# Kernel optimization log

Hardware: AMD Instinct MI355X
Metric: run time of the kernel (lower is better)

Reference implementation:

```python
import jax, jax.numpy as jnp
import numpy as np

D = 256; HEADS = 8; LEVELS = 4; POINTS = 4; DFFN = 1024
B = 8; NQ = 300; NC = 16
SPATIAL = [(64, 64), (32, 32), (16, 16), (8, 8)]  # (H, W) per feature level (static)
LEN_IN = sum(h * w for h, w in SPATIAL)  # 5440
EPS = 1e-5


def layer_norm(x, w, b):
    m = x.mean(-1, keepdims=True)
    v = ((x - m) ** 2).mean(-1, keepdims=True)
    return (x - m) * jax.lax.rsqrt(v + EPS) * w + b


def mha(q, k, v, in_w, in_b, out_w, out_b):
    # torch nn.MultiheadAttention with packed qkv in_proj. q,k,v: [b, s, D]
    b, s, _ = q.shape
    dh = D // HEADS
    wq, wk, wv = jnp.split(in_w, 3, axis=0)
    bq, bk, bv = jnp.split(in_b, 3)
    proj = lambda x, w, bb: (x @ w.T + bb).reshape(b, s, HEADS, dh).transpose(0, 2, 1, 3)
    qh, kh, vh = proj(q, wq, bq), proj(k, wk, bk), proj(v, wv, bv)
    attn = jax.nn.softmax(jnp.einsum('bhqd,bhkd->bhqk', qh / np.sqrt(dh), kh), axis=-1)
    o = jnp.einsum('bhqk,bhkd->bhqd', attn, vh).transpose(0, 2, 1, 3).reshape(b, s, D)
    return o @ out_w.T + out_b


def bilinear_sample(value_l, loc, H_, W_):
    # value_l: [b, heads, H_*W_, dh]; loc: [b, heads, lq, P, 2] normalized to [0,1]
    # matches F.grid_sample(mode='bilinear', padding_mode='zeros', align_corners=False)
    b, nh, lq, p, _ = loc.shape
    dh = value_l.shape[-1]
    x = loc[..., 0] * W_ - 0.5
    y = loc[..., 1] * H_ - 0.5
    x0f = jnp.floor(x); y0f = jnp.floor(y)
    lx = x - x0f; ly = y - y0f
    x0 = x0f.astype(jnp.int32); y0 = y0f.astype(jnp.int32)
    def gather(xi, yi, w):
        valid = (xi >= 0) & (xi < W_) & (yi >= 0) & (yi < H_)
        idx = jnp.clip(yi, 0, H_ - 1) * W_ + jnp.clip(xi, 0, W_ - 1)
        vals = jnp.take_along_axis(value_l, idx.reshape(b, nh, lq * p, 1), axis=2)
        return vals.reshape(b, nh, lq, p, dh) * (w * valid)[..., None]
    out = gather(x0, y0, (1 - lx) * (1 - ly))
    out = out + gather(x0 + 1, y0, lx * (1 - ly))
    out = out + gather(x0, y0 + 1, (1 - lx) * ly)
    out = out + gather(x0 + 1, y0 + 1, lx * ly)
    return out  # [b, heads, lq, P, dh]


def ms_deform_attn(query, ref_pts, src, pad_mask, value_w, value_b, off_w, off_b, attw_w, attw_b, out_w, out_b):
    b, lq, _ = query.shape
    dh = D // HEADS
    value = src @ value_w.T + value_b
    value = jnp.where(pad_mask[..., None], 0.0, value)
    value = value.reshape(b, LEN_IN, HEADS, dh).transpose(0, 2, 1, 3)  # [b,H,Len,dh]
    off = (query @ off_w.T + off_b).reshape(b, lq, HEADS, LEVELS, POINTS, 2)
    aw = jax.nn.softmax((query @ attw_w.T + attw_b).reshape(b, lq, HEADS, LEVELS * POINTS), axis=-1)
    aw = aw.reshape(b, lq, HEADS, LEVELS, POINTS).transpose(0, 2, 1, 3, 4)  # [b,H,lq,L,P]
    norm = jnp.array([[w_, h_] for h_, w_ in SPATIAL], dtype=query.dtype)  # (W, H) per level
    loc = ref_pts[:, :, None, :, None, :] + off / norm[None, None, None, :, None, :]
    loc = loc.transpose(0, 2, 1, 3, 4, 5)  # [b,H,lq,L,P,2]
    out = jnp.zeros((b, HEADS, lq, dh), query.dtype)
    start = 0
    for l, (H_, W_) in enumerate(SPATIAL):
        v_l = jax.lax.dynamic_slice_in_dim(value, start, H_ * W_, axis=2)
        s = bilinear_sample(v_l, loc[:, :, :, l], H_, W_)
        out = out + (s * aw[:, :, :, l, :, None]).sum(3)
        start += H_ * W_
    out = out.transpose(0, 2, 1, 3).reshape(b, lq, D)
    return out @ out_w.T + out_b


def setup_inputs():
    ks = iter(jax.random.split(jax.random.key(0), 64))
    w = lambda *shape: jax.random.normal(next(ks), shape, jnp.float32) * 0.02
    return {
        'tgt': jax.random.normal(next(ks), (B, NQ, NC, D), jnp.float32),
        'query_pos': jax.random.normal(next(ks), (B, NQ, NC, D), jnp.float32),
        'reference_points': jax.random.uniform(next(ks), (B, NQ * NC, LEVELS, 2), jnp.float32),
        'src': jax.random.normal(next(ks), (B, LEN_IN, D), jnp.float32),
        'src_spatial_shapes': jnp.array(SPATIAL, jnp.int32),
        'level_start_index': jnp.array(np.cumsum([0] + [h * ww for h, ww in SPATIAL[:-1]]), jnp.int32),
        'src_padding_mask': jnp.zeros((B, LEN_IN), bool),
        'sa_in_w': w(3 * D, D), 'sa_in_b': jnp.zeros(3 * D, jnp.float32),
        'sa_out_w': w(D, D), 'sa_out_b': jnp.zeros(D, jnp.float32),
        'norm2_w': jnp.ones(D, jnp.float32), 'norm2_b': jnp.zeros(D, jnp.float32),
        'ca_value_w': w(D, D), 'ca_value_b': jnp.zeros(D, jnp.float32),
        'ca_off_w': w(HEADS * LEVELS * POINTS * 2, D), 'ca_off_b': w(HEADS * LEVELS * POINTS * 2),
        'ca_attw_w': w(HEADS * LEVELS * POINTS, D), 'ca_attw_b': jnp.zeros(HEADS * LEVELS * POINTS, jnp.float32),
        'ca_out_w': w(D, D), 'ca_out_b': jnp.zeros(D, jnp.float32),
        'norm1_w': jnp.ones(D, jnp.float32), 'norm1_b': jnp.zeros(D, jnp.float32),
        'lin1_w': w(DFFN, D), 'lin1_b': jnp.zeros(DFFN, jnp.float32),
        'lin2_w': w(D, DFFN), 'lin2_b': jnp.zeros(D, jnp.float32),
        'norm3_w': jnp.ones(D, jnp.float32), 'norm3_b': jnp.zeros(D, jnp.float32),
    }


def _forward(tgt, query_pos, reference_points, src, pad_mask, sa_in_w, sa_in_b, sa_out_w, sa_out_b, norm2_w, norm2_b, ca_value_w, ca_value_b, ca_off_w, ca_off_b, ca_attw_w, ca_attw_b, ca_out_w, ca_out_b, norm1_w, norm1_b, lin1_w, lin1_b, lin2_w, lin2_b, norm3_w, norm3_b):
    b, nq, nc, dm = tgt.shape
    # point-to-point self-attention within each contour (batch folded with queries)
    t = tgt.reshape(b * nq, nc, dm)
    qp = query_pos.reshape(b * nq, nc, dm)
    q = t + qp
    t2 = mha(q, q, t, sa_in_w, sa_in_b, sa_out_w, sa_out_b)
    t = layer_norm(t + t2, norm2_w, norm2_b)
    # multi-scale deformable cross-attention over flattened feature pyramid
    t = t.reshape(b, nq * nc, dm)
    qp = qp.reshape(b, nq * nc, dm)
    t2 = ms_deform_attn(t + qp, reference_points, src, pad_mask, ca_value_w, ca_value_b, ca_off_w, ca_off_b, ca_attw_w, ca_attw_b, ca_out_w, ca_out_b)
    t = layer_norm(t + t2, norm1_w, norm1_b)
    # FFN (dropout is identity in eval)
    t2 = jax.nn.relu(t @ lin1_w.T + lin1_b) @ lin2_w.T + lin2_b
    t = layer_norm(t + t2, norm3_w, norm3_b)
    return t.reshape(b, nq, nc, dm)


def reference(tgt, query_pos, reference_points, src, src_spatial_shapes, level_start_index, src_padding_mask, sa_in_w, sa_in_b, sa_out_w, sa_out_b, norm2_w, norm2_b, ca_value_w, ca_value_b, ca_off_w, ca_off_b, ca_attw_w, ca_attw_b, ca_out_w, ca_out_b, norm1_w, norm1_b, lin1_w, lin1_b, lin2_w, lin2_b, norm3_w, norm3_b):
    # src_spatial_shapes / level_start_index are static (SPATIAL); accepted for API fidelity
    return _forward(tgt, query_pos, reference_points, src, src_padding_mask, sa_in_w, sa_in_b, sa_out_w, sa_out_b, norm2_w, norm2_b, ca_value_w, ca_value_b, ca_off_w, ca_off_b, ca_attw_w, ca_attw_b, ca_out_w, ca_out_b, norm1_w, norm1_b, lin1_w, lin1_b, lin2_w, lin2_b, norm3_w, norm3_b)
```

## Files before the change

kernel.cpp:

```cpp
#include <hip/hip_runtime.h>


typedef __bf16 bf16x8 __attribute__((ext_vector_type(8)));
typedef float  f32x4  __attribute__((ext_vector_type(4)));
typedef float  f32x2  __attribute__((ext_vector_type(2)));

__device__ __forceinline__ unsigned pk_bf16(float lo, float hi)
{
    unsigned a = __float_as_uint(lo) + 0x8000u;
    unsigned b = __float_as_uint(hi) + 0x8000u;
    return __builtin_amdgcn_perm(b, a, 0x07060302u);
}
__device__ __forceinline__ unsigned short f2bf(float v)
{
    return (unsigned short)((__float_as_uint(v) + 0x8000u) >> 16);
}
__device__ __forceinline__ float bf_lo(unsigned u) { return __uint_as_float(u << 16); }
__device__ __forceinline__ float bf_hi(unsigned u) { return __uint_as_float(u & 0xffff0000u); }
__device__ __forceinline__ float bf1(unsigned short u) { return __uint_as_float((unsigned)u << 16); }
__device__ __forceinline__ f32x2 bfpair(unsigned u)
{
    f32x2 r;
    r.x = __uint_as_float(u << 16);
    r.y = __uint_as_float(u & 0xffff0000u);
    return r;
}

struct WcvtArgs {
    const float* src[8];
    unsigned short* dst[8];
    int n4[8];
};

__global__ __launch_bounds__(256) void wcvt(WcvtArgs a)
{
    const int gid = blockIdx.x * 256 + threadIdx.x;
    const int stride = gridDim.x * 256;
#pragma unroll
    for (int s = 0; s < 8; s++) {
        const float4* sp = (const float4*)a.src[s];
        uint2* dp = (uint2*)a.dst[s];
        for (int i = gid; i < a.n4[s]; i += stride) {
            float4 f = sp[i];
            uint2 o; o.x = pk_bf16(f.x, f.y); o.y = pk_bf16(f.z, f.w);
            dp[i] = o;
        }
    }
}

template <int ABF16>
__device__ __forceinline__ void gemm_core64(
    const void* __restrict__ Xv, const float* __restrict__ Y,
    const unsigned short* __restrict__ Wb, const float* __restrict__ bias,
    void* __restrict__ Cv, int outbf16, int relu,
    int row0, int col0, int N, int K,
    unsigned short (*sA)[64][40], unsigned short (*sB)[128][40])
{
    const int tid  = threadIdx.x;
    const int lane = tid & 63;
    const int wv   = tid >> 6;
    const int wr   = wv >> 1;
    const int wc   = wv & 1;
    const int lm   = lane & 15;
    const int ko   = (lane >> 4) << 3;
    const int q4   = (lane >> 4) << 2;

    const int ar  = tid >> 2;
    const int ash = (tid & 3) << 3;
    const int br  = tid >> 1;
    const int bsh = (tid & 1) << 4;

    const unsigned short* Ab = (const unsigned short*)Xv;
    const float* Af = (const float*)Xv;

    f32x4 acc[2][4] = {};
    uint4 ra, rb0, rb1;

    const int iters = K >> 5;

    auto load_k = [&](int k) {
        if (ABF16) {
            ra = *(const uint4*)(Ab + (size_t)(row0 + ar) * K + k + ash);
        } else {
            const float* Ar = Af + (size_t)(row0 + ar) * K + k + ash;
            float4 f0 = ((const float4*)Ar)[0];
            float4 f1 = ((const float4*)Ar)[1];
            if (Y) {
                const float* Yr = Y + (size_t)(row0 + ar) * K + k + ash;
                float4 g0 = ((const float4*)Yr)[0];
                float4 g1 = ((const float4*)Yr)[1];
                f0.x += g0.x; f0.y += g0.y; f0.z += g0.z; f0.w += g0.w;
                f1.x += g1.x; f1.y += g1.y; f1.z += g1.z; f1.w += g1.w;
            }
            ra.x = pk_bf16(f0.x, f0.y); ra.y = pk_bf16(f0.z, f0.w);
            ra.z = pk_bf16(f1.x, f1.y); ra.w = pk_bf16(f1.z, f1.w);
        }
        const unsigned short* Wr = Wb + (size_t)(col0 + br) * K + k + bsh;
        rb0 = ((const uint4*)Wr)[0];
        rb1 = ((const uint4*)Wr)[1];
    };
    auto store_k = [&](int buf) {
        *(uint4*)&sA[buf][ar][ash]     = ra;
        *(uint4*)&sB[buf][br][bsh]     = rb0;
        *(uint4*)&sB[buf][br][bsh + 8] = rb1;
    };

    load_k(0);
    store_k(0);

    for (int it = 0; it < iters; ++it) {
        __syncthreads();
        const int buf = it & 1;
        if (it + 1 < iters) load_k((it + 1) << 5);

        bf16x8 av[2], bv[4];
#pragma unroll
        for (int mi = 0; mi < 2; mi++)
            av[mi] = *(const bf16x8*)&sA[buf][wr * 32 + mi * 16 + lm][ko];
#pragma unroll
        for (int ni = 0; ni < 4; ni++)
            bv[ni] = *(const bf16x8*)&sB[buf][wc * 64 + ni * 16 + lm][ko];
#pragma unroll
        for (int mi = 0; mi < 2; mi++)
#pragma unroll
            for (int ni = 0; ni < 4; ni++)
                acc[mi][ni] = __builtin_amdgcn_mfma_f32_16x16x32_bf16(
                    av[mi], bv[ni], acc[mi][ni], 0, 0, 0);

        if (it + 1 < iters) store_k(buf ^ 1);
    }

#pragma unroll
    for (int ni = 0; ni < 4; ni++) {
        const int col = col0 + wc * 64 + ni * 16 + lm;
        const float bsv = bias[col];
#pragma unroll
        for (int mi = 0; mi < 2; mi++) {
            const int rowb = row0 + wr * 32 + mi * 16 + q4;
#pragma unroll
            for (int rr = 0; rr < 4; rr++) {
                float v = acc[mi][ni][rr] + bsv;
                if (relu) v = fmaxf(v, 0.f);
                if (outbf16)
                    ((unsigned short*)Cv)[(size_t)(rowb + rr) * N + col] = f2bf(v);
                else
                    ((float*)Cv)[(size_t)(rowb + rr) * N + col] = v;
            }
        }
    }
}

template <int ABF16>
__global__ __launch_bounds__(256) void gemm_std64(
    const void* __restrict__ Xv, const float* __restrict__ Y,
    const unsigned short* __restrict__ Wb, const float* __restrict__ bias,
    void* __restrict__ Cv, int outbf16, int relu, int N, int K)
{
    __shared__ unsigned short sA[2][64][40];
    __shared__ unsigned short sB[2][128][40];
    gemm_core64<ABF16>(Xv, Y, Wb, bias, Cv, outbf16, relu,
                       blockIdx.y * 64, blockIdx.x * 128, N, K, sA, sB);
}

__global__ __launch_bounds__(256) void gemm_qkvval(
    const float* __restrict__ tgt, const float* __restrict__ qpos,
    const unsigned short* __restrict__ Wsa, const float* __restrict__ bsa,
    unsigned short* __restrict__ qkB, unsigned short* __restrict__ vB,
    const float* __restrict__ src,
    const unsigned short* __restrict__ Wval, const float* __restrict__ bval,
    unsigned short* __restrict__ valB)
{
    __shared__ unsigned short sA[2][64][40];
    __shared__ unsigned short sB[2][128][40];
    const int x = blockIdx.x, y = blockIdx.y;
    if (x < 4) {
        if (y >= 600) return;
        gemm_core64<0>(tgt, qpos, Wsa, bsa, qkB, 1, 0, y * 64, x * 128, 512, 256, sA, sB);
    } else if (x < 6) {
        if (y >= 600) return;
        gemm_core64<0>(tgt, nullptr, Wsa + 512 * 256, bsa + 512, vB, 1, 0,
                       y * 64, (x - 4) * 128, 256, 256, sA, sB);
    } else {
        gemm_core64<0>(src, nullptr, Wval, bval, valB, 1, 0,
                       y * 64, (x - 6) * 128, 256, 256, sA, sB);
    }
}

__global__ __launch_bounds__(256) void gemm_offaw(
    const unsigned short* __restrict__ X,
    const unsigned short* __restrict__ Woff, const float* __restrict__ boff,
    unsigned short* __restrict__ offB,
    const unsigned short* __restrict__ Watt, const float* __restrict__ batt,
    float* __restrict__ awL)
{
    __shared__ unsigned short sA[2][64][40];
    __shared__ unsigned short sB[2][128][40];
    if (blockIdx.x >= 2)
        gemm_core64<1>(X, nullptr, Watt, batt, awL, 0, 0,
                       blockIdx.y * 64, 0, 128, 256, sA, sB);
    else
        gemm_core64<1>(X, nullptr, Woff, boff, offB, 1, 0,
                       blockIdx.y * 64, blockIdx.x * 128, 256, 256, sA, sB);
}

__global__ __launch_bounds__(256) void attn16(
    const unsigned short* __restrict__ QK, const unsigned short* __restrict__ V,
    unsigned short* __restrict__ O)
{
    __shared__ unsigned short sqk[16][520];
    __shared__ unsigned short sv[16][264];
    __shared__ float sp[128][17];

    const int g = blockIdx.x;
    const int tid = threadIdx.x;

    const uint4* qg = (const uint4*)(QK + (size_t)g * 8192);
    for (int i = tid; i < 1024; i += 256)
        *(uint4*)&sqk[i >> 6][(i & 63) * 8] = qg[i];
    const uint4* vg = (const uint4*)(V + (size_t)g * 4096);
    for (int i = tid; i < 512; i += 256)
        *(uint4*)&sv[i >> 5][(i & 31) * 8] = vg[i];
    __syncthreads();

#pragma unroll 2
    for (int s = tid; s < 2048; s += 256) {
        const int h = s >> 8, qi = (s >> 4) & 15, kj = s & 15;
        const uint4* qp = (const uint4*)&sqk[qi][h * 32];
        const uint4* kp = (const uint4*)&sqk[kj][256 + h * 32];
        float acc = 0.f;
#pragma unroll
        for (int c = 0; c < 4; c++) {
            uint4 qu = qp[c];
            uint4 ku = kp[c];
            acc += bf_lo(qu.x) * bf_lo(ku.x) + bf_hi(qu.x) * bf_hi(ku.x)
                 + bf_lo(qu.y) * bf_lo(ku.y) + bf_hi(qu.y) * bf_hi(ku.y)
                 + bf_lo(qu.z) * bf_lo(ku.z) + bf_hi(qu.z) * bf_hi(ku.z)
                 + bf_lo(qu.w) * bf_lo(ku.w) + bf_hi(qu.w) * bf_hi(ku.w);
        }
        sp[s >> 4][s & 15] = acc * 0.17677669529663687f;
    }
    __syncthreads();

    if (tid < 128) {
        float* row = sp[tid];
        float mx = row[0];
#pragma unroll
        for (int j = 1; j < 16; j++) mx = fmaxf(mx, row[j]);
        float sum = 0.f;
#pragma unroll
        for (int j = 0; j < 16; j++) { float e = __expf(row[j] - mx); row[j] = e; sum += e; }
        float inv = 1.f / sum;
#pragma unroll
        for (int j = 0; j < 16; j++) row[j] *= inv;
    }
    __syncthreads();

    uint2* og = (uint2*)(O + (size_t)g * 4096);
    for (int o = tid; o < 1024; o += 256) {
        const int qi = o >> 6, cq = o & 63, h = cq >> 3;
        const float* pr = sp[h * 16 + qi];
        float a0 = 0.f, a1 = 0.f, a2 = 0.f, a3 = 0.f;
#pragma unroll
        for (int j = 0; j < 16; j++) {
            uint2 u = *(const uint2*)&sv[j][cq * 4];
            float p = pr[j];
            a0 += p * bf_lo(u.x); a1 += p * bf_hi(u.x);
            a2 += p * bf_lo(u.y); a3 += p * bf_hi(u.y);
        }
        uint2 r; r.x = pk_bf16(a0, a1); r.y = pk_bf16(a2, a3);
        og[o] = r;
    }
}

template <int XBF16, int WRITE2, int ADDQ>
__global__ __launch_bounds__(256) void ln_res4(
    const void* __restrict__ Xv, const float* __restrict__ R,
    const float* __restrict__ w, const float* __restrict__ b,
    float* __restrict__ out, unsigned short* __restrict__ out2,
    const float* __restrict__ qpos)
{
    const int row = blockIdx.x * 4 + (threadIdx.x >> 6);
    const int lane = threadIdx.x & 63;
    const size_t base = (size_t)row * 256 + lane * 4;

    float x0, x1, x2, x3;
    if (XBF16) {
        uint2 u = *(const uint2*)((const unsigned short*)Xv + base);
        x0 = bf_lo(u.x); x1 = bf_hi(u.x); x2 = bf_lo(u.y); x3 = bf_hi(u.y);
    } else {
        float4 f = *(const float4*)((const float*)Xv + base);
        x0 = f.x; x1 = f.y; x2 = f.z; x3 = f.w;
    }
    float4 r4 = *(const float4*)&R[base];
    float v0 = x0 + r4.x, v1 = x1 + r4.y, v2 = x2 + r4.z, v3 = x3 + r4.w;

    float s = v0 + v1 + v2 + v3;
#pragma unroll
    for (int o = 32; o > 0; o >>= 1) s += __shfl_xor(s, o);
    const float mean = s * (1.f / 256.f);
    const float d0 = v0 - mean, d1 = v1 - mean, d2 = v2 - mean, d3 = v3 - mean;
    float q = d0 * d0 + d1 * d1 + d2 * d2 + d3 * d3;
#pragma unroll
    for (int o = 32; o > 0; o >>= 1) q += __shfl_xor(q, o);
    const float rs = rsqrtf(q * (1.f / 256.f) + 1e-5f);

    float4 w4 = *(const float4*)&w[lane * 4];
    float4 b4 = *(const float4*)&b[lane * 4];
    float y0 = d0 * rs * w4.x + b4.x;
    float y1 = d1 * rs * w4.y + b4.y;
    float y2 = d2 * rs * w4.z + b4.z;
    float y3 = d3 * rs * w4.w + b4.w;

    float4 o4; o4.x = y0; o4.y = y1; o4.z = y2; o4.w = y3;
    *(float4*)&out[base] = o4;
    if (WRITE2) {
        float z0 = y0, z1 = y1, z2 = y2, z3 = y3;
        if (ADDQ) {
            float4 qp4 = *(const float4*)&qpos[base];
            z0 += qp4.x; z1 += qp4.y; z2 += qp4.z; z3 += qp4.w;
        }
        uint2 u; u.x = pk_bf16(z0, z1); u.y = pk_bf16(z2, z3);
        *(uint2*)(out2 + base) = u;
    }
}

__global__ __launch_bounds__(256) void ms_sample4(
    const unsigned short* __restrict__ VAL, const unsigned short* __restrict__ OFF,
    const float* __restrict__ AWL, const float* __restrict__ REF,
    unsigned short* __restrict__ OUT)
{
    __shared__ unsigned short soff[1024];
    __shared__ float saw[512];
    __shared__ float sref[32];
    __shared__ float swt[4][16][8][4];
    __shared__ int   sidx[4][16][8][4];

    const int m0 = blockIdx.x * 4, tid = threadIdx.x;

    ((uint2*)soff)[tid] = ((const uint2*)(OFF + (size_t)m0 * 256))[tid];
    ((float2*)saw)[tid] = ((const float2*)(AWL + (size_t)m0 * 128))[tid];
    if (tid < 32) sref[tid] = REF[(size_t)m0 * 8 + tid];
    __syncthreads();

    if (tid < 32) {
        float* row = &saw[tid * 16];
        float mx = row[0];
#pragma unroll
        for (int j = 1; j < 16; j++) mx = fmaxf(mx, row[j]);
        float s = 0.f, e[16];
#pragma unroll
        for (int j = 0; j < 16; j++) { e[j] = __expf(row[j] - mx); s += e[j]; }
        float inv = 1.f / s;
#pragma unroll
        for (int j = 0; j < 16; j++) row[j] = e[j] * inv;
    }
    __syncthreads();

    for (int c = tid; c < 512; c += 256) {
        const int qi = c >> 7, h = c & 7, j = (c >> 3) & 15;
        const int l = j >> 2, p = j & 3;
        const int Wl = 64 >> l;
        const int st = (l == 0) ? 0 : (l == 1) ? 4096 : (l == 2) ? 5120 : 5376;
        const float fS = (float)Wl;
        const unsigned short* ob = &soff[qi * 256 + h * 32 + l * 8 + p * 2];
        const float x = sref[qi * 8 + l * 2 + 0] * fS + bf1(ob[0]) - 0.5f;
        const float y = sref[qi * 8 + l * 2 + 1] * fS + bf1(ob[1]) - 0.5f;
        const float x0f = floorf(x), y0f = floorf(y);
        const float fx = x - x0f, fy = y - y0f;
        const int x0 = (int)x0f, y0 = (int)y0f;
        const int x1 = x0 + 1, y1 = y0 + 1;
        const float vx0 = (x0 >= 0 && x0 < Wl) ? 1.f : 0.f;
        const float vx1 = (x1 >= 0 && x1 < Wl) ? 1.f : 0.f;
        const float vy0 = (y0 >= 0 && y0 < Wl) ? 1.f : 0.f;
        const float vy1 = (y1 >= 0 && y1 < Wl) ? 1.f : 0.f;
        const int cx0 = min(max(x0, 0), Wl - 1);
        const int cx1 = min(max(x1, 0), Wl - 1);
        const int cy0 = min(max(y0, 0), Wl - 1);
        const int cy1 = min(max(y1, 0), Wl - 1);
        const float aw = saw[qi * 128 + h * 16 + j];
        float4 w4;
        w4.x = (1.f - fx) * (1.f - fy) * vx0 * vy0 * aw;
        w4.y = fx * (1.f - fy) * vx1 * vy0 * aw;
        w4.z = (1.f - fx) * fy * vx0 * vy1 * aw;
        w4.w = fx * fy * vx1 * vy1 * aw;
        int4 i4;
        i4.x = (st + cy0 * Wl + cx0) << 9;
        i4.y = (st + cy0 * Wl + cx1) << 9;
        i4.z = (st + cy1 * Wl + cx0) << 9;
        i4.w = (st + cy1 * Wl + cx1) << 9;
        *(float4*)&swt[qi][j][h][0] = w4;
        *(int4*)&sidx[qi][j][h][0]  = i4;
    }
    __syncthreads();

    const int qi = tid >> 6, lane = tid & 63, h = lane >> 3;
    const int m = m0 + qi, bb = m / 4800;
    const char* vb = (const char*)VAL + (size_t)bb * 5440 * 512 + lane * 8;

    f32x2 a01 = {0.f, 0.f}, a23 = {0.f, 0.f};
#pragma unroll 4
    for (int j = 0; j < 16; j++) {
        const float4 w = *(const float4*)&swt[qi][j][h][0];
        const int4  id = *(const int4*)&sidx[qi][j][h][0];
        uint2 c0 = *(const uint2*)(vb + id.x);
        uint2 c1 = *(const uint2*)(vb + id.y);
        uint2 c2 = *(const uint2*)(vb + id.z);
        uint2 c3 = *(const uint2*)(vb + id.w);
        a01 += w.x * bfpair(c0.x) + w.y * bfpair(c1.x)
             + w.z * bfpair(c2.x) + w.w * bfpair(c3.x);
        a23 += w.x * bfpair(c0.y) + w.y * bfpair(c1.y)
             + w.z * bfpair(c2.y) + w.w * bfpair(c3.y);
    }
    uint2 o;
    o.x = pk_bf16(a01.x, a01.y);
    o.y = pk_bf16(a23.x, a23.y);
    *(uint2*)(OUT + (size_t)m * 256 + lane * 4) = o;
}

extern "C" void kernel_launch(void* const* d_in, const int* in_sizes, int n_in,
                              void* d_out, int out_size, void* d_ws, size_t ws_size,
                              hipStream_t stream)
{
    const float* tgt        = (const float*)d_in[0];
    const float* qpos       = (const float*)d_in[1];
    const float* refp       = (const float*)d_in[2];
    const float* src        = (const float*)d_in[3];
    const float* sa_in_w    = (const float*)d_in[7];
    const float* sa_in_b    = (const float*)d_in[8];
    const float* sa_out_w   = (const float*)d_in[9];
    const float* sa_out_b   = (const float*)d_in[10];
    const float* norm2_w    = (const float*)d_in[11];
    const float* norm2_b    = (const float*)d_in[12];
    const float* ca_value_w = (const float*)d_in[13];
    const float* ca_value_b = (const float*)d_in[14];
    const float* ca_off_w   = (const float*)d_in[15];
    const float* ca_off_b   = (const float*)d_in[16];
    const float* ca_attw_w  = (const float*)d_in[17];
    const float* ca_attw_b  = (const float*)d_in[18];
    const float* ca_out_w   = (const float*)d_in[19];
    const float* ca_out_b   = (const float*)d_in[20];
    const float* norm1_w    = (const float*)d_in[21];
    const float* norm1_b    = (const float*)d_in[22];
    const float* lin1_w     = (const float*)d_in[23];
    const float* lin1_b     = (const float*)d_in[24];
    const float* lin2_w     = (const float*)d_in[25];
    const float* lin2_b     = (const float*)d_in[26];
    const float* norm3_w    = (const float*)d_in[27];
    const float* norm3_b    = (const float*)d_in[28];
    float* out = (float*)d_out;

    const int M1 = 38400;
    float* ws = (float*)d_ws;
    float* A  = ws;
    float* Bx = A  + 9830400;
    float* Cx = Bx + 4915200;
    float* Dx = Cx + 4915200;
    float* Ex = Dx + 4915200;
    float* Fx = Ex + 5570560;
    float* Gx = Fx + 19660800;

    unsigned short* qkB   = (unsigned short*)A;
    float*          t1    = A;
    float*          t2    = A;
    unsigned short* vB    = (unsigned short*)Bx;
    unsigned short* t1qB  = (unsigned short*)Bx;
    unsigned short* sampB = (unsigned short*)Bx;
    unsigned short* l2B   = (unsigned short*)Bx;
    unsigned short* aoB   = (unsigned short*)Cx;
    unsigned short* offB  = (unsigned short*)Cx;
    unsigned short* coB   = (unsigned short*)Cx;
    unsigned short* t2B   = (unsigned short*)Cx;
    unsigned short* soB   = (unsigned short*)Dx;
    float*          awL   = Dx;
    unsigned short* valB  = (unsigned short*)Ex;
    unsigned short* hidB  = (unsigned short*)Fx;
    unsigned short* wG    = (unsigned short*)Gx;

    unsigned short* wSAIN  = wG;
    unsigned short* wSAOUT = wG + 196608;
    unsigned short* wVAL   = wG + 262144;
    unsigned short* wOFF   = wG + 327680;
    unsigned short* wATT   = wG + 393216;
    unsigned short* wCAOUT = wG + 425984;
    unsigned short* wL1    = wG + 491520;
    unsigned short* wL2    = wG + 753664;

    dim3 blk(256);

    WcvtArgs wa;
    wa.src[0] = sa_in_w;    wa.dst[0] = wSAIN;  wa.n4[0] = 196608 / 4;
    wa.src[1] = sa_out_w;   wa.dst[1] = wSAOUT; wa.n4[1] = 65536 / 4;
    wa.src[2] = ca_value_w; wa.dst[2] = wVAL;   wa.n4[2] = 65536 / 4;
    wa.src[3] = ca_off_w;   wa.dst[3] = wOFF;   wa.n4[3] = 65536 / 4;
    wa.src[4] = ca_attw_w;  wa.dst[4] = wATT;   wa.n4[4] = 32768 / 4;
    wa.src[5] = ca_out_w;   wa.dst[5] = wCAOUT; wa.n4[5] = 65536 / 4;
    wa.src[6] = lin1_w;     wa.dst[6] = wL1;    wa.n4[6] = 262144 / 4;
    wa.src[7] = lin2_w;     wa.dst[7] = wL2;    wa.n4[7] = 262144 / 4;
    wcvt<<<512, blk, 0, stream>>>(wa);

    gemm_qkvval<<<dim3(8, 680), blk, 0, stream>>>(tgt, qpos, wSAIN, sa_in_b, qkB, vB,
                                                  src, wVAL, ca_value_b, valB);
    attn16<<<2400, blk, 0, stream>>>(qkB, vB, aoB);
    gemm_std64<1><<<dim3(2, 600), blk, 0, stream>>>(aoB, nullptr, wSAOUT, sa_out_b, soB, 1, 0, 256, 256);
    ln_res4<1, 1, 1><<<9600, blk, 0, stream>>>(soB, tgt, norm2_w, norm2_b, t1, t1qB, qpos);

    gemm_offaw<<<dim3(3, 600), blk, 0, stream>>>(t1qB, wOFF, ca_off_b, offB, wATT, ca_attw_b, awL);
    ms_sample4<<<9600, blk, 0, stream>>>(valB, offB, awL, refp, sampB);
    gemm_std64<1><<<dim3(2, 600), blk, 0, stream>>>(sampB, nullptr, wCAOUT, ca_out_b, coB, 1, 0, 256, 256);
    ln_res4<1, 1, 0><<<9600, blk, 0, stream>>>(coB, t1, norm1_w, norm1_b, t2, t2B, nullptr);

    gemm_std64<1><<<dim3(8, 600), blk, 0, stream>>>(t2B, nullptr, wL1, lin1_b, hidB, 1, 1, 1024, 256);
    gemm_std64<1><<<dim3(2, 600), blk, 0, stream>>>(hidB, nullptr, wL2, lin2_b, l2B, 1, 0, 256, 1024);
    ln_res4<1, 0, 0><<<9600, blk, 0, stream>>>(l2B, t2, norm3_w, norm3_b, out, nullptr, nullptr);
}
```

Before: 589.5 us.

## Replace tiled GEMMs with A-stationary row-block GEMM streaming weights from global

Replaces the double-buffered 64x128 LDS-tiled GEMM with a kernel that stages a 64-row slab of A (256-wide K chunk) in shared memory once, keeps it in registers, and loops over output column groups while loading B fragments directly from global/L2. This removes repeated A re-reads across column blocks and most of the per-k synchronisation, and cuts grid size to one block per row slab. In exchange, weights are read uncached by LDS per wave with less latency hiding, each wave handles only 16 rows, and blocks serialize over column groups, reducing parallelism.

After: 1.080 ms. 1.83x slower.

```diff
diff --git a/kernel.cpp b/kernel.cpp
--- a/kernel.cpp
+++ b/kernel.cpp
@@ -48,98 +48,66 @@
     }
 }
 
-template <int ABF16>
-__device__ __forceinline__ void gemm_core64(
+template <int ABF16, int NF, int KC>
+__device__ __forceinline__ void gemm_astat(
     const void* __restrict__ Xv, const float* __restrict__ Y,
     const unsigned short* __restrict__ Wb, const float* __restrict__ bias,
     void* __restrict__ Cv, int outbf16, int relu,
-    int row0, int col0, int N, int K,
-    unsigned short (*sA)[64][40], unsigned short (*sB)[128][40])
+    int row0, int N, int groups, unsigned short (*sA)[264])
 {
     const int tid  = threadIdx.x;
     const int lane = tid & 63;
     const int wv   = tid >> 6;
-    const int wr   = wv >> 1;
-    const int wc   = wv & 1;
     const int lm   = lane & 15;
     const int ko   = (lane >> 4) << 3;
     const int q4   = (lane >> 4) << 2;
-
-    const int ar  = tid >> 2;
-    const int ash = (tid & 3) << 3;
-    const int br  = tid >> 1;
-    const int bsh = (tid & 1) << 4;
-
-    const unsigned short* Ab = (const unsigned short*)Xv;
-    const float* Af = (const float*)Xv;
-
-    f32x4 acc[2][4] = {};
-    uint4 ra, rb0, rb1;
-
-    const int iters = K >> 5;
-
-    auto load_k = [&](int k) {
+    const int K    = KC * 256;
+
+    const int arow = tid >> 2;
+    const int aseg = tid & 3;
+
+    auto stage = [&](int kc) {
+        uint4* dst = (uint4*)&sA[arow][aseg * 64];
         if (ABF16) {
-            ra = *(const uint4*)(Ab + (size_t)(row0 + ar) * K + k + ash);
+            const uint4* Ar = (const uint4*)((const unsigned short*)Xv +
+                              (size_t)(row0 + arow) * K + kc * 256 + aseg * 64);
+#pragma unroll
+            for (int i = 0; i < 8; i++) {
+                const int j = (i + aseg) & 7;
+                dst[j] = Ar[j];
+            }
         } else {
-            const float* Ar = Af + (size_t)(row0 + ar) * K + k + ash;
-            float4 f0 = ((const float4*)Ar)[0];
-            float4 f1 = ((const float4*)Ar)[1];
-            if (Y) {
-                const float* Yr = Y + (size_t)(row0 + ar) * K + k + ash;
-                float4 g0 = ((const float4*)Yr)[0];
-                float4 g1 = ((const float4*)Yr)[1];
-                f0.x += g0.x; f0.y += g0.y; f0.z += g0.z; f0.w += g0.w;
-                f1.x += g1.x; f1.y += g1.y; f1.z += g1.z; f1.w += g1.w;
+            const float* Ar = (const float*)Xv + (size_t)(row0 + arow) * 256 + aseg * 64;
+            const float* Yr = Y ? (Y + (size_t)(row0 + arow) * 256 + aseg * 64) : nullptr;
+#pragma unroll
+            for (int i = 0; i < 8; i++) {
+                const int j = (i + aseg) & 7;
+                float4 f0 = ((const float4*)Ar)[2 * j];
+                float4 f1 = ((const float4*)Ar)[2 * j + 1];
+                if (Y) {
+                    float4 g0 = ((const float4*)Yr)[2 * j];
+                    float4 g1 = ((const float4*)Yr)[2 * j + 1];
+                    f0.x += g0.x; f0.y += g0.y; f0.z += g0.z; f0.w += g0.w;
+                    f1.x += g1.x; f1.y += g1.y; f1.z += g1.z; f1.w += g1.w;
+                }
+                uint4 u;
+                u.x = pk_bf16(f0.x, f0.y); u.y = pk_bf16(f0.z, f0.w);
+                u.z = pk_bf16(f1.x, f1.y); u.w = pk_bf16(f1.z, f1.w);
+                dst[j] = u;
             }
-            ra.x = pk_bf16(f0.x, f0.y); ra.y = pk_bf16(f0.z, f0.w);
-            ra.z = pk_bf16(f1.x, f1.y); ra.w = pk_bf16(f1.z, f1.w);
-        }
-        const unsigned short* Wr = Wb + (size_t)(col0 + br) * K + k + bsh;
-        rb0 = ((const uint4*)Wr)[0];
-        rb1 = ((const uint4*)Wr)[1];
+        }
     };
-    auto store_k = [&](int buf) {
-        *(uint4*)&sA[buf][ar][ash]     = ra;
-        *(uint4*)&sB[buf][br][bsh]     = rb0;
-        *(uint4*)&sB[buf][br][bsh + 8] = rb1;
-    };
-
-    load_k(0);
-    store_k(0);
-
-    for (int it = 0; it < iters; ++it) {
-        __syncthreads();
-        const int buf = it & 1;
-        if (it + 1 < iters) load_k((it + 1) << 5);
-
-        bf16x8 av[2], bv[4];
-#pragma unroll
-        for (int mi = 0; mi < 2; mi++)
-            av[mi] = *(const bf16x8*)&sA[buf][wr * 32 + mi * 16 + lm][ko];
-#pragma unroll
-        for (int ni = 0; ni < 4; ni++)
-            bv[ni] = *(const bf16x8*)&sB[buf][wc * 64 + ni * 16 + lm][ko];
-#pragma unroll
-        for (int mi = 0; mi < 2; mi++)
-#pragma unroll
-            for (int ni = 0; ni < 4; ni++)
-                acc[mi][ni] = __builtin_amdgcn_mfma_f32_16x16x32_bf16(
-                    av[mi], bv[ni], acc[mi][ni], 0, 0, 0);
-
-        if (it + 1 < iters) store_k(buf ^ 1);
-    }
-
-#pragma unroll
-    for (int ni = 0; ni < 4; ni++) {
-        const int col = col0 + wc * 64 + ni * 16 + lm;
-        const float bsv = bias[col];
-#pragma unroll
-        for (int mi = 0; mi < 2; mi++) {
-            const int rowb = row0 + wr * 32 + mi * 16 + q4;
+
+    const int rowb = row0 + wv * 16 + q4;
+
+    auto epi = [&](f32x4* acc, int colg) {
+#pragma unroll
+        for (int nf = 0; nf < NF; nf++) {
+            const int col = colg + nf * 16 + lm;
+            const float bsv = bias[col];
 #pragma unroll
             for (int rr = 0; rr < 4; rr++) {
-                float v = acc[mi][ni][rr] + bsv;
+                float v = acc[nf][rr] + bsv;
                 if (relu) v = fmaxf(v, 0.f);
                 if (outbf16)
                     ((unsigned short*)Cv)[(size_t)(rowb + rr) * N + col] = f2bf(v);
@@ -147,19 +115,69 @@
                     ((float*)Cv)[(size_t)(rowb + rr) * N + col] = v;
             }
         }
-    }
-}
-
-template <int ABF16>
-__global__ __launch_bounds__(256) void gemm_std64(
+    };
+
+    if (KC == 1) {
+        stage(0);
+        __syncthreads();
+        bf16x8 av[8];
+#pragma unroll
+        for (int ks = 0; ks < 8; ks++)
+            av[ks] = *(const bf16x8*)&sA[wv * 16 + lm][ks * 32 + ko];
+
+        for (int g = 0; g < groups; g++) {
+            const int colg = g * (NF * 16);
+            f32x4 acc[NF] = {};
+#pragma unroll
+            for (int nf = 0; nf < NF; nf++) {
+                const unsigned short* Wr = Wb + (size_t)(colg + nf * 16 + lm) * K + ko;
+                bf16x8 bv[8];
+#pragma unroll
+                for (int ks = 0; ks < 8; ks++)
+                    bv[ks] = *(const bf16x8*)(Wr + ks * 32);
+#pragma unroll
+                for (int ks = 0; ks < 8; ks++)
+                    acc[nf] = __builtin_amdgcn_mfma_f32_16x16x32_bf16(
+                        av[ks], bv[ks], acc[nf], 0, 0, 0);
+            }
+            epi(acc, colg);
+        }
+    } else {
+        f32x4 acc[NF] = {};
+        for (int kc = 0; kc < KC; kc++) {
+            if (kc) __syncthreads();
+            stage(kc);
+            __syncthreads();
+            bf16x8 av[8];
+#pragma unroll
+            for (int ks = 0; ks < 8; ks++)
+                av[ks] = *(const bf16x8*)&sA[wv * 16 + lm][ks * 32 + ko];
+#pragma unroll
+            for (int nf = 0; nf < NF; nf++) {
+                const unsigned short* Wr = Wb + (size_t)(nf * 16 + lm) * K + kc * 256 + ko;
+                bf16x8 bv[8];
+#pragma unroll
+                for (int ks = 0; ks < 8; ks++)
+                    bv[ks] = *(const bf16x8*)(Wr + ks * 32);
+#pragma unroll
+                for (int ks = 0; ks < 8; ks++)
+                    acc[nf] = __builtin_amdgcn_mfma_f32_16x16x32_bf16(
+                        av[ks], bv[ks], acc[nf], 0, 0, 0);
+            }
+        }
+        epi(acc, 0);
+    }
+}
+
+template <int ABF16, int NF, int KC>
+__global__ __launch_bounds__(256) void gemm_one(
     const void* __restrict__ Xv, const float* __restrict__ Y,
     const unsigned short* __restrict__ Wb, const float* __restrict__ bias,
-    void* __restrict__ Cv, int outbf16, int relu, int N, int K)
-{
-    __shared__ unsigned short sA[2][64][40];
-    __shared__ unsigned short sB[2][128][40];
-    gemm_core64<ABF16>(Xv, Y, Wb, bias, Cv, outbf16, relu,
-                       blockIdx.y * 64, blockIdx.x * 128, N, K, sA, sB);
+    void* __restrict__ Cv, int outbf16, int relu, int N, int groups)
+{
+    __shared__ unsigned short sA[64][264];
+    gemm_astat<ABF16, NF, KC>(Xv, Y, Wb, bias, Cv, outbf16, relu,
+                              blockIdx.x * 64, N, groups, sA);
 }
 
 __global__ __launch_bounds__(256) void gemm_qkvval(
@@ -170,20 +188,16 @@
     const unsigned short* __restrict__ Wval, const float* __restrict__ bval,
     unsigned short* __restrict__ valB)
 {
-    __shared__ unsigned short sA[2][64][40];
-    __shared__ unsigned short sB[2][128][40];
-    const int x = blockIdx.x, y = blockIdx.y;
-    if (x < 4) {
-        if (y >= 600) return;
-        gemm_core64<0>(tgt, qpos, Wsa, bsa, qkB, 1, 0, y * 64, x * 128, 512, 256, sA, sB);
-    } else if (x < 6) {
-        if (y >= 600) return;
-        gemm_core64<0>(tgt, nullptr, Wsa + 512 * 256, bsa + 512, vB, 1, 0,
-                       y * 64, (x - 4) * 128, 256, 256, sA, sB);
-    } else {
-        gemm_core64<0>(src, nullptr, Wval, bval, valB, 1, 0,
-                       y * 64, (x - 6) * 128, 256, 256, sA, sB);
-    }
+    __shared__ unsigned short sA[64][264];
+    const int b = blockIdx.x;
+    if (b < 600)
+        gemm_astat<0, 8, 1>(tgt, qpos, Wsa, bsa, qkB, 1, 0, b * 64, 512, 4, sA);
+    else if (b < 1200)
+        gemm_astat<0, 8, 1>(tgt, nullptr, Wsa + 512 * 256, bsa + 512, vB, 1, 0,
+                            (b - 600) * 64, 256, 2, sA);
+    else
+        gemm_astat<0, 8, 1>(src, nullptr, Wval, bval, valB, 1, 0,
+                            (b - 1200) * 64, 256, 2, sA);
 }
 
 __global__ __launch_bounds__(256) void gemm_offaw(
@@ -193,14 +207,12 @@
     const unsigned short* __restrict__ Watt, const float* __restrict__ batt,
     float* __restrict__ awL)
 {
-    __shared__ unsigned short sA[2][64][40];
-    __shared__ unsigned short sB[2][128][40];
-    if (blockIdx.x >= 2)
-        gemm_core64<1>(X, nullptr, Watt, batt, awL, 0, 0,
-                       blockIdx.y * 64, 0, 128, 256, sA, sB);
+    __shared__ unsigned short sA[64][264];
+    const int b = blockIdx.x;
+    if (b < 600)
+        gemm_astat<1, 8, 1>(X, nullptr, Woff, boff, offB, 1, 0, b * 64, 256, 2, sA);
     else
-        gemm_core64<1>(X, nullptr, Woff, boff, offB, 1, 0,
-                       blockIdx.y * 64, blockIdx.x * 128, 256, 256, sA, sB);
+        gemm_astat<1, 8, 1>(X, nullptr, Watt, batt, awL, 0, 0, (b - 600) * 64, 128, 1, sA);
 }
 
 __global__ __launch_bounds__(256) void attn16(
@@ -449,7 +461,6 @@
     const float* norm3_b    = (const float*)d_in[28];
     float* out = (float*)d_out;
 
-    const int M1 = 38400;
     float* ws = (float*)d_ws;
     float* A  = ws;
     float* Bx = A  + 9830400;
@@ -498,18 +509,18 @@
     wa.src[7] = lin2_w;     wa.dst[7] = wL2;    wa.n4[7] = 262144 / 4;
     wcvt<<<512, blk, 0, stream>>>(wa);
 
-    gemm_qkvval<<<dim3(8, 680), blk, 0, stream>>>(tgt, qpos, wSAIN, sa_in_b, qkB, vB,
-                                                  src, wVAL, ca_value_b, valB);
+    gemm_qkvval<<<1880, blk, 0, stream>>>(tgt, qpos, wSAIN, sa_in_b, qkB, vB,
+                                          src, wVAL, ca_value_b, valB);
     attn16<<<2400, blk, 0, stream>>>(qkB, vB, aoB);
-    gemm_std64<1><<<dim3(2, 600), blk, 0, stream>>>(aoB, nullptr, wSAOUT, sa_out_b, soB, 1, 0, 256, 256);
+    gemm_one<1, 8, 1><<<600, blk, 0, stream>>>(aoB, nullptr, wSAOUT, sa_out_b, soB, 1, 0, 256, 2);
     ln_res4<1, 1, 1><<<9600, blk, 0, stream>>>(soB, tgt, norm2_w, norm2_b, t1, t1qB, qpos);
 
-    gemm_offaw<<<dim3(3, 600), blk, 0, stream>>>(t1qB, wOFF, ca_off_b, offB, wATT, ca_attw_b, awL);
+    gemm_offaw<<<1200, blk, 0, stream>>>(t1qB, wOFF, ca_off_b, offB, wATT, ca_attw_b, awL);
     ms_sample4<<<9600, blk, 0, stream>>>(valB, offB, awL, refp, sampB);
-    gemm_std64<1><<<dim3(2, 600), blk, 0, stream>>>(sampB, nullptr, wCAOUT, ca_out_b, coB, 1, 0, 256, 256);
+    gemm_one<1, 8, 1><<<600, blk, 0, stream>>>(sampB, nullptr, wCAOUT, ca_out_b, coB, 1, 0, 256, 2);
     ln_res4<1, 1, 0><<<9600, blk, 0, stream>>>(coB, t1, norm1_w, norm1_b, t2, t2B, nullptr);
 
-    gemm_std64<1><<<dim3(8, 600), blk, 0, stream>>>(t2B, nullptr, wL1, lin1_b, hidB, 1, 1, 1024, 256);
-    gemm_std64<1><<<dim3(2, 600), blk, 0, stream>>>(hidB, nullptr, wL2, lin2_b, l2B, 1, 0, 256, 1024);
+    gemm_one<1, 8, 1><<<600, blk, 0, stream>>>(t2B, nullptr, wL1, lin1_b, hidB, 1, 1, 1024, 8);
+    gemm_one<1, 16, 4><<<600, blk, 0, stream>>>(hidB, nullptr, wL2, lin2_b, l2B, 1, 0, 256, 1);
     ln_res4<1, 0, 0><<<9600, blk, 0, stream>>>(l2B, t2, norm3_w, norm3_b, out, nullptr, nullptr);
 }
```
